# Kernel optimization log

Measured on AMD Instinct MI355X. Metric: run time of the kernel, lower is better.

The kernel has to match this reference:

```python
import jax, jax.numpy as jnp
import numpy as np

NHEAD, HD, ITERS = 8, 32, 6


def _layernorm(x, g, b, eps=1e-5):
    mu = jnp.mean(x, axis=-1, keepdims=True)
    var = jnp.mean((x - mu) ** 2, axis=-1, keepdims=True)
    return g * (x - mu) / jnp.sqrt(var + eps) + b


def _msa1(x, ax, WQ, bQ, WK, bK, WV, bV, WO, bO):
    # ring (sliding-window, size 3) attention + relay node as 4th key/value
    B, L, H = x.shape
    q = (x @ WQ + bQ).reshape(B, L, NHEAD, HD)
    k = (x @ WK + bK).reshape(B, L, NHEAD, HD)
    ak = (ax @ WK + bK).reshape(B, 1, NHEAD, 1, HD)   # relay key
    av = (ax @ WV + bV).reshape(B, 1, NHEAD, 1, HD)   # relay value
    padk = jnp.pad(k, ((0, 0), (1, 1), (0, 0), (0, 0)))
    wins = jnp.stack([padk[:, t:L + t] for t in range(3)], axis=3)  # [B,L,nh,3,hd]
    ak_b = jnp.broadcast_to(ak, (B, L, NHEAD, 1, HD))
    av_b = jnp.broadcast_to(av, (B, L, NHEAD, 1, HD))
    keys = jnp.concatenate([ak_b, wins], axis=3)   # [B,L,nh,4,hd]
    # NOTE: faithful to source bug: window VALUES come from k (pad_v = F.pad(k,...))
    vals = jnp.concatenate([av_b, wins], axis=3)
    scores = jnp.einsum('blnd,blnkd->blnk', q, keys) / np.sqrt(HD).astype(np.float32)
    alphas = jax.nn.softmax(scores, axis=-1)
    att = jnp.einsum('blnk,blnkd->blnd', alphas, vals).reshape(B, L, NHEAD * HD)
    return att @ WO + bO


def _msa2(x, y, WQ, bQ, WK, bK, WV, bV, WO, bO):
    # relay attends over [relay; nodes]; mask arg is ignored in the original
    B, L1, H = y.shape
    q = (x @ WQ + bQ).reshape(B, NHEAD, HD)
    k = (y @ WK + bK).reshape(B, L1, NHEAD, HD)
    v = (y @ WV + bV).reshape(B, L1, NHEAD, HD)
    scores = jnp.einsum('bnd,blnd->bnl', q, k) / np.sqrt(HD).astype(np.float32)
    alphas = jax.nn.softmax(scores, axis=-1)
    att = jnp.einsum('bnl,blnd->bnd', alphas, v).reshape(B, NHEAD * HD)
    return att @ WO + bO


def setup_inputs() -> dict:
    key = jax.random.key(0)
    ks = jax.random.split(key, 32)
    B, L, H, V, E, I = 32, 512, 256, 32000, 300, 6

    def rn(k, shape, s=0.05):
        return jax.random.normal(k, shape, jnp.float32) * s

    inp = {
        'data': jax.random.randint(ks[0], (B, L), 0, V),
        'emb': rn(ks[1], (V, E), 0.1),
        'emb_fc_W': rn(ks[2], (E, H)),
        'emb_fc_b': jnp.zeros((H,), jnp.float32),
        'pos_emb': rn(ks[3], (1000, H), 0.02),
        'ln_g': jnp.ones((I, H), jnp.float32),
        'ln_b': jnp.zeros((I, H), jnp.float32),
    }
    names = ['r_WQ', 'r_WK', 'r_WV', 'r_WO', 's_WQ', 's_WK', 's_WV', 's_WO']
    for j, n in enumerate(names):
        inp[n] = rn(ks[4 + j], (I, H, H))
        inp[n.replace('W', 'b')] = rn(ks[12 + j], (I, H), 0.01)
    return inp


def reference(data, emb, emb_fc_W, emb_fc_b, pos_emb, ln_g, ln_b,
              r_WQ, r_bQ, r_WK, r_bK, r_WV, r_bV, r_WO, r_bO,
              s_WQ, s_bQ, s_WK, s_bK, s_WV, s_bV, s_WO, s_bO):
    B, L = data.shape
    mask = (data == 1)
    e = emb[data]                                  # [B,L,nemb]
    P = pos_emb[:L][None]                          # [1,L,H]
    x0 = e @ emb_fc_W + emb_fc_b + P               # [B,L,H]
    nodes = x0
    relay = jnp.mean(x0, axis=1)                   # [B,H]
    for i in range(ITERS):
        ax = relay
        n_ln = _layernorm(nodes, ln_g[i], ln_b[i])
        nodes = nodes + jax.nn.leaky_relu(
            _msa1(n_ln, ax, r_WQ[i], r_bQ[i], r_WK[i], r_bK[i],
                  r_WV[i], r_bV[i], r_WO[i], r_bO[i]))
        y = jnp.concatenate([relay[:, None, :], nodes], axis=1)
        relay = jax.nn.leaky_relu(
            _msa2(relay, y, s_WQ[i], s_bQ[i], s_WK[i], s_bK[i],
                  s_WV[i], s_bV[i], s_WO[i], s_bO[i]))
        nodes = jnp.where(mask[:, :, None], 0.0, nodes)
    rep = 0.5 * jnp.max(nodes, axis=1) + 0.5 * relay
    return rep
```

## Files before the change

### kernel.cpp

```cpp
#include <hip/hip_runtime.h>
#include <stdint.h>

typedef __bf16 bf16x8 __attribute__((ext_vector_type(8)));
typedef unsigned short ushort8 __attribute__((ext_vector_type(8)));
typedef float floatx4 __attribute__((ext_vector_type(4)));

__device__ __forceinline__ unsigned short f2b(float f) {
    unsigned int u = __builtin_bit_cast(unsigned int, f);
    u += 0x7fffu + ((u >> 16) & 1u);
    return (unsigned short)(u >> 16);
}
__device__ __forceinline__ float b2f(unsigned short u) {
    union { unsigned int i; float f; } x; x.i = ((unsigned int)u) << 16; return x.f;
}

#define SCALE_QK 0.17677669529663687f

__global__ void transpose_many(const float* __restrict__ w0,
                               const float* __restrict__ w1,
                               const float* __restrict__ w2,
                               const float* __restrict__ w3,
                               const float* __restrict__ w4,
                               unsigned short* __restrict__ out) {
    int m = blockIdx.y;
    int fam = m / 6, it = m % 6;
    const float* src =
        (fam == 0 ? w0 : fam == 1 ? w1 : fam == 2 ? w2 : fam == 3 ? w3 : w4) + it * 65536;
    int e = blockIdx.x * 256 + threadIdx.x;
    int n = e >> 8, k = e & 255;
    out[(size_t)(it * 5 + fam) * 65536 + e] = f2b(src[k * 256 + n]);
}

__global__ void transpose_emb(const float* __restrict__ W,
                              unsigned short* __restrict__ out) {
    int e = blockIdx.x * 256 + threadIdx.x;
    int n = e / 320, k = e % 320;
    out[e] = (k < 300) ? f2b(W[k * 256 + n]) : (unsigned short)0;
}

__global__ void gather_emb(const int* __restrict__ data,
                           const float* __restrict__ emb,
                           unsigned short* __restrict__ apad) {
    int row = blockIdx.x;
    int tok = data[row];
    const float* er = emb + (size_t)tok * 300;
    for (int c = threadIdx.x; c < 320; c += 256)
        apad[(size_t)row * 320 + c] = (c < 300) ? f2b(er[c]) : (unsigned short)0;
}

template <int EPI>
__global__ __launch_bounds__(256) void gemm_k(const unsigned short* __restrict__ A, int K,
                                              const unsigned short* __restrict__ Bt,
                                              const float* __restrict__ bias0,
                                              const float* __restrict__ bias1,
                                              float* __restrict__ outF,
                                              unsigned short* __restrict__ outB0,
                                              unsigned short* __restrict__ outB1,
                                              const float* __restrict__ pos,
                                              const int* __restrict__ dmask,
                                              int applyMask) {
    __shared__ unsigned short Asm[64 * 72];
    __shared__ unsigned short Bsm[64 * 72];
    const int tid = threadIdx.x;
    const int wave = tid >> 6, lane = tid & 63;
    const int wm = (wave >> 1) * 32, wn = (wave & 1) * 32;
    const int quad = lane >> 4, l16 = lane & 15;
    const int rowBase = blockIdx.x * 64, colBase = blockIdx.y * 64;
    const int sRow = tid >> 2, sCol = (tid & 3) * 8;
    const unsigned short* aG = A + (size_t)(rowBase + sRow) * K + sCol;
    const unsigned short* bG = Bt + (size_t)(colBase + sRow) * K + sCol;

    floatx4 acc[2][2] = {};
    for (int k0 = 0; k0 < K; k0 += 64) {
        uint4 a0 = *(const uint4*)(aG + k0);
        uint4 a1 = *(const uint4*)(aG + k0 + 32);
        uint4 b0 = *(const uint4*)(bG + k0);
        uint4 b1 = *(const uint4*)(bG + k0 + 32);
        __syncthreads();
        *(uint4*)&Asm[sRow * 72 + sCol] = a0;
        *(uint4*)&Asm[sRow * 72 + sCol + 32] = a1;
        *(uint4*)&Bsm[sRow * 72 + sCol] = b0;
        *(uint4*)&Bsm[sRow * 72 + sCol + 32] = b1;
        __syncthreads();
#pragma unroll
        for (int kk = 0; kk < 64; kk += 32) {
            bf16x8 af0 = __builtin_bit_cast(bf16x8, *(const ushort8*)&Asm[(wm + l16) * 72 + kk + quad * 8]);
            bf16x8 af1 = __builtin_bit_cast(bf16x8, *(const ushort8*)&Asm[(wm + 16 + l16) * 72 + kk + quad * 8]);
            bf16x8 bf0 = __builtin_bit_cast(bf16x8, *(const ushort8*)&Bsm[(wn + l16) * 72 + kk + quad * 8]);
            bf16x8 bf1 = __builtin_bit_cast(bf16x8, *(const ushort8*)&Bsm[(wn + 16 + l16) * 72 + kk + quad * 8]);
            acc[0][0] = __builtin_amdgcn_mfma_f32_16x16x32_bf16(af0, bf0, acc[0][0], 0, 0, 0);
            acc[0][1] = __builtin_amdgcn_mfma_f32_16x16x32_bf16(af0, bf1, acc[0][1], 0, 0, 0);
            acc[1][0] = __builtin_amdgcn_mfma_f32_16x16x32_bf16(af1, bf0, acc[1][0], 0, 0, 0);
            acc[1][1] = __builtin_amdgcn_mfma_f32_16x16x32_bf16(af1, bf1, acc[1][1], 0, 0, 0);
        }
    }
    const int group = colBase >> 8;
    const float* bias = (EPI == 0 && group) ? bias1 : bias0;
    unsigned short* obf = (EPI == 0 && group) ? outB1 : outB0;
#pragma unroll
    for (int tm = 0; tm < 2; tm++) {
#pragma unroll
        for (int tn = 0; tn < 2; tn++) {
            int col = colBase + wn + tn * 16 + l16;
            int lc = col & 255;
            float bv = bias[lc];
#pragma unroll
            for (int r = 0; r < 4; r++) {
                int row = rowBase + wm + tm * 16 + quad * 4 + r;
                float c = acc[tm][tn][r] + bv;
                size_t o = (size_t)row * 256 + lc;
                if (EPI == 0) {
                    obf[o] = f2b(c);
                } else if (EPI == 1) {
                    float v = c > 0.f ? c : 0.01f * c;
                    float base = outF[o];
                    if (applyMask && dmask[row] == 1) base = 0.f;
                    float rr = base + v;
                    outF[o] = rr;
                    outB0[o] = f2b(rr);
                } else {
                    outF[o] = c + pos[(row & 511) * 256 + lc];
                }
            }
        }
    }
}

__global__ void mean_part(const float* __restrict__ nodes, float* __restrict__ part) {
    int b = blockIdx.x, c = blockIdx.y, h = threadIdx.x;
    const float* p = nodes + ((size_t)b * 512 + c * 32) * 256 + h;
    float s = 0.f;
    for (int l = 0; l < 32; l++) s += p[l * 256];
    part[(b * 16 + c) * 256 + h] = s;
}
__global__ void mean_comb(const float* __restrict__ part, float* __restrict__ relay) {
    int b = blockIdx.x, h = threadIdx.x;
    float s = 0.f;
    for (int c = 0; c < 16; c++) s += part[(b * 16 + c) * 256 + h];
    relay[b * 256 + h] = s * (1.f / 512.f);
}

__global__ __launch_bounds__(256) void ln_k(const float* __restrict__ nodes,
                                            const float* __restrict__ g,
                                            const float* __restrict__ bb,
                                            unsigned short* __restrict__ out,
                                            const int* __restrict__ dmask,
                                            int applyMask) {
    __shared__ float red[8];
    int row = blockIdx.x, t = threadIdx.x;
    int wv = t >> 6, ln_ = t & 63;
    float x = nodes[(size_t)row * 256 + t];
    if (applyMask && dmask[row] == 1) x = 0.f;
    float s = x;
#pragma unroll
    for (int o = 32; o; o >>= 1) s += __shfl_xor(s, o);
    if (ln_ == 0) red[wv] = s;
    __syncthreads();
    float mu = (red[0] + red[1] + red[2] + red[3]) * (1.f / 256.f);
    float d = x - mu;
    float v = d * d;
#pragma unroll
    for (int o = 32; o; o >>= 1) v += __shfl_xor(v, o);
    if (ln_ == 0) red[4 + wv] = v;
    __syncthreads();
    float var = (red[4] + red[5] + red[6] + red[7]) * (1.f / 256.f);
    float inv = rsqrtf(var + 1e-5f);
    out[(size_t)row * 256 + t] = f2b(g[t] * d * inv + bb[t]);
}

__global__ void relay5(const float* __restrict__ relay,
                       const float* __restrict__ rWK, const float* __restrict__ rbK,
                       const float* __restrict__ rWV, const float* __restrict__ rbV,
                       const float* __restrict__ sWQ, const float* __restrict__ sbQ,
                       const float* __restrict__ sWK, const float* __restrict__ sbK,
                       const float* __restrict__ sWV, const float* __restrict__ sbV,
                       float* __restrict__ AK, float* __restrict__ AV,
                       float* __restrict__ Q2, float* __restrict__ RK2, float* __restrict__ RV2) {
    __shared__ float r[256];
    int b = blockIdx.x, fam = blockIdx.y, t = threadIdx.x;
    r[t] = relay[b * 256 + t];
    __syncthreads();
    const float* W; const float* bi; float* o;
    switch (fam) {
        case 0: W = rWK; bi = rbK; o = AK; break;
        case 1: W = rWV; bi = rbV; o = AV; break;
        case 2: W = sWQ; bi = sbQ; o = Q2; break;
        case 3: W = sWK; bi = sbK; o = RK2; break;
        default: W = sWV; bi = sbV; o = RV2; break;
    }
    float s = 0.f;
    for (int e = 0; e < 256; e++) s += r[e] * W[e * 256 + t];
    o[b * 256 + t] = s + bi[t];
}

__global__ __launch_bounds__(256) void attn1_k(const unsigned short* __restrict__ q,
                                               const unsigned short* __restrict__ k,
                                               const float* __restrict__ ak,
                                               const float* __restrict__ av,
                                               unsigned short* __restrict__ att) {
    int row = blockIdx.x;
    int b = row >> 9, l = row & 511;
    int t = threadIdx.x;
    size_t o = (size_t)row * 256 + t;
    float qv = b2f(q[o]);
    float k0v = b2f(k[o]);
    float km = (l > 0) ? b2f(k[o - 256]) : 0.f;
    float kp = (l < 511) ? b2f(k[o + 256]) : 0.f;
    float akv = ak[b * 256 + t], avv = av[b * 256 + t];
    float s0 = qv * akv, s1 = qv * km, s2 = qv * k0v, s3 = qv * kp;
#pragma unroll
    for (int off = 16; off; off >>= 1) {
        s0 += __shfl_xor(s0, off, 32);
        s1 += __shfl_xor(s1, off, 32);
        s2 += __shfl_xor(s2, off, 32);
        s3 += __shfl_xor(s3, off, 32);
    }
    s0 *= SCALE_QK; s1 *= SCALE_QK; s2 *= SCALE_QK; s3 *= SCALE_QK;
    float m = fmaxf(fmaxf(s0, s1), fmaxf(s2, s3));
    float e0 = __expf(s0 - m), e1 = __expf(s1 - m), e2 = __expf(s2 - m), e3 = __expf(s3 - m);
    float Z = e0 + e1 + e2 + e3;
    float a = (e0 * avv + e1 * km + e2 * k0v + e3 * kp) / Z;
    att[o] = f2b(a);
}

__global__ __launch_bounds__(256) void attn2_k(const float* __restrict__ q2,
                                               const unsigned short* __restrict__ k2,
                                               const unsigned short* __restrict__ v2,
                                               const float* __restrict__ rk2,
                                               const float* __restrict__ rv2,
                                               float* __restrict__ att2) {
    __shared__ float sc[513];
    __shared__ float qs[32];
    __shared__ float red[16];
    __shared__ float red2[256];
    int bn = blockIdx.x;
    int b = bn >> 3, n = bn & 7;
    int t = threadIdx.x;
    if (t < 32) qs[t] = q2[b * 256 + n * 32 + t];
    __syncthreads();
    float lmax = -1e30f;
    for (int li = t; li < 513; li += 256) {
        float d = 0.f;
        if (li == 0) {
            const float* kr = rk2 + b * 256 + n * 32;
#pragma unroll 8
            for (int j = 0; j < 32; j++) d += qs[j] * kr[j];
        } else {
            const unsigned short* kr = k2 + ((size_t)(b * 512 + li - 1) * 256 + n * 32);
#pragma unroll 8
            for (int j = 0; j < 32; j++) d += qs[j] * b2f(kr[j]);
        }
        d *= SCALE_QK;
        sc[li] = d;
        lmax = fmaxf(lmax, d);
    }
#pragma unroll
    for (int o = 32; o; o >>= 1) lmax = fmaxf(lmax, __shfl_xor(lmax, o));
    if ((t & 63) == 0) red[t >> 6] = lmax;
    __syncthreads();
    float m = fmaxf(fmaxf(red[0], red[1]), fmaxf(red[2], red[3]));
    float lsum = 0.f;
    for (int li = t; li < 513; li += 256) {
        float e = __expf(sc[li] - m);
        sc[li] = e;
        lsum += e;
    }
#pragma unroll
    for (int o = 32; o; o >>= 1) lsum += __shfl_xor(lsum, o);
    if ((t & 63) == 0) red[8 + (t >> 6)] = lsum;
    __syncthreads();
    float Z = red[8] + red[9] + red[10] + red[11];
    int d_ = t & 31, g_ = t >> 5;
    float acc = 0.f;
    for (int li = g_; li < 513; li += 8) {
        if (li == 0) {
            acc += sc[0] * rv2[b * 256 + n * 32 + d_];
        } else {
            acc += sc[li] * b2f(v2[(size_t)(b * 512 + li - 1) * 256 + n * 32 + d_]);
        }
    }
    red2[t] = acc;
    __syncthreads();
    if (t < 32) {
        float s = 0.f;
        for (int g = 0; g < 8; g++) s += red2[g * 32 + t];
        att2[b * 256 + n * 32 + t] = s / Z;
    }
}

__global__ void relay_out2(const float* __restrict__ att2,
                           const float* __restrict__ WO, const float* __restrict__ bO,
                           float* __restrict__ relay) {
    __shared__ float r[256];
    int b = blockIdx.x, t = threadIdx.x;
    r[t] = att2[b * 256 + t];
    __syncthreads();
    float s = 0.f;
    for (int e = 0; e < 256; e++) s += r[e] * WO[e * 256 + t];
    s += bO[t];
    relay[b * 256 + t] = s > 0.f ? s : 0.01f * s;
}

__global__ void rep_part(const float* __restrict__ nodes, const int* __restrict__ dmask,
                         float* __restrict__ part) {
    int b = blockIdx.x, c = blockIdx.y, h = threadIdx.x;
    const float* p = nodes + ((size_t)b * 512 + c * 32) * 256 + h;
    const int* dd = dmask + b * 512 + c * 32;
    float m = -1e30f;
    for (int l = 0; l < 32; l++) {
        float v = (dd[l] == 1) ? 0.f : p[l * 256];
        m = fmaxf(m, v);
    }
    part[(b * 16 + c) * 256 + h] = m;
}
__global__ void rep_comb(const float* __restrict__ part, const float* __restrict__ relay,
                         float* __restrict__ out) {
    int b = blockIdx.x, h = threadIdx.x;
    float m = -1e30f;
    for (int c = 0; c < 16; c++) m = fmaxf(m, part[(b * 16 + c) * 256 + h]);
    out[b * 256 + h] = 0.5f * m + 0.5f * relay[b * 256 + h];
}

extern "C" void kernel_launch(void* const* d_in, const int* in_sizes, int n_in,
                              void* d_out, int out_size, void* d_ws, size_t ws_size,
                              hipStream_t stream) {
    const int* data = (const int*)d_in[0];
    const float* emb = (const float*)d_in[1];
    const float* emb_fc_W = (const float*)d_in[2];
    const float* emb_fc_b = (const float*)d_in[3];
    const float* pos_emb = (const float*)d_in[4];
    const float* ln_g = (const float*)d_in[5];
    const float* ln_b = (const float*)d_in[6];
    const float* r_WQ = (const float*)d_in[7];
    const float* r_bQ = (const float*)d_in[8];
    const float* r_WK = (const float*)d_in[9];
    const float* r_bK = (const float*)d_in[10];
    const float* r_WV = (const float*)d_in[11];
    const float* r_bV = (const float*)d_in[12];
    const float* r_WO = (const float*)d_in[13];
    const float* r_bO = (const float*)d_in[14];
    const float* s_WQ = (const float*)d_in[15];
    const float* s_bQ = (const float*)d_in[16];
    const float* s_WK = (const float*)d_in[17];
    const float* s_bK = (const float*)d_in[18];
    const float* s_WV = (const float*)d_in[19];
    const float* s_bV = (const float*)d_in[20];
    const float* s_WO = (const float*)d_in[21];
    const float* s_bO = (const float*)d_in[22];

    char* w = (char*)d_ws;
    size_t off = 0;
    auto alloc = [&](size_t bytes) -> char* {
        char* p = w + off;
        off += (bytes + 255) & ~(size_t)255;
        return p;
    };
    float* RELAY = (float*)alloc(8192 * 4);
    float* AK = (float*)alloc(8192 * 4);
    float* AV = (float*)alloc(8192 * 4);
    float* Q2 = (float*)alloc(8192 * 4);
    float* RK2 = (float*)alloc(8192 * 4);
    float* RV2 = (float*)alloc(8192 * 4);
    float* ATT2 = (float*)alloc(8192 * 4);
    float* PART = (float*)alloc((size_t)32 * 16 * 256 * 4);
    unsigned short* WTE = (unsigned short*)alloc((size_t)256 * 320 * 2);
    unsigned short* WT = (unsigned short*)alloc((size_t)30 * 65536 * 2);
    float* NODES = (float*)alloc((size_t)16384 * 256 * 4);
    unsigned short* NLN = (unsigned short*)alloc((size_t)16384 * 256 * 2);
    unsigned short* Qb = (unsigned short*)alloc((size_t)16384 * 256 * 2);
    unsigned short* Kb16 = (unsigned short*)alloc((size_t)16384 * 256 * 2);
    unsigned short* NBF = (unsigned short*)alloc((size_t)16384 * 320 * 2);
    unsigned short* AEMB = NBF;
    unsigned short* ATT = NLN;
    unsigned short* K2b = Qb;
    unsigned short* V2b = Kb16;

    transpose_many<<<dim3(256, 30), 256, 0, stream>>>(r_WQ, r_WK, r_WO, s_WK, s_WV, WT);
    transpose_emb<<<320, 256, 0, stream>>>(emb_fc_W, WTE);
    gather_emb<<<16384, 256, 0, stream>>>(data, emb, AEMB);
    gemm_k<2><<<dim3(256, 4), 256, 0, stream>>>(AEMB, 320, WTE, emb_fc_b, nullptr,
                                                NODES, nullptr, nullptr, pos_emb, nullptr, 0);
    mean_part<<<dim3(32, 16), 256, 0, stream>>>(NODES, PART);
    mean_comb<<<32, 256, 0, stream>>>(PART, RELAY);

    for (int i = 0; i < 6; i++) {
        const unsigned short* wQK = WT + (size_t)(i * 5 + 0) * 65536;
        const unsigned short* wO = WT + (size_t)(i * 5 + 2) * 65536;
        const unsigned short* wKV2 = WT + (size_t)(i * 5 + 3) * 65536;

        ln_k<<<16384, 256, 0, stream>>>(NODES, ln_g + i * 256, ln_b + i * 256, NLN, data, i > 0);
        gemm_k<0><<<dim3(256, 8), 256, 0, stream>>>(NLN, 256, wQK, r_bQ + i * 256, r_bK + i * 256,
                                                    nullptr, Qb, Kb16, nullptr, nullptr, 0);
        relay5<<<dim3(32, 5), 256, 0, stream>>>(RELAY,
                                                r_WK + (size_t)i * 65536, r_bK + i * 256,
                                                r_WV + (size_t)i * 65536, r_bV + i * 256,
                                                s_WQ + (size_t)i * 65536, s_bQ + i * 256,
                                                s_WK + (size_t)i * 65536, s_bK + i * 256,
                                                s_WV + (size_t)i * 65536, s_bV + i * 256,
                                                AK, AV, Q2, RK2, RV2);
        attn1_k<<<16384, 256, 0, stream>>>(Qb, Kb16, AK, AV, ATT);
        gemm_k<1><<<dim3(256, 4), 256, 0, stream>>>(ATT, 256, wO, r_bO + i * 256, nullptr,
                                                    NODES, NBF, nullptr, nullptr, data, i > 0);
        gemm_k<0><<<dim3(256, 8), 256, 0, stream>>>(NBF, 256, wKV2, s_bK + i * 256, s_bV + i * 256,
                                                    nullptr, K2b, V2b, nullptr, nullptr, 0);
        attn2_k<<<256, 256, 0, stream>>>(Q2, K2b, V2b, RK2, RV2, ATT2);
        relay_out2<<<32, 256, 0, stream>>>(ATT2, s_WO + (size_t)i * 65536, s_bO + i * 256, RELAY);
    }
    rep_part<<<dim3(32, 16), 256, 0, stream>>>(NODES, data, PART);
    rep_comb<<<32, 256, 0, stream>>>(PART, RELAY, (float*)d_out);
}
```

Before: 858.9 us.

## Load full-K GEMM tiles via direct global-to-LDS with XOR swizzle; vectorize attn1

```diff
diff --git a/kernel.cpp b/kernel.cpp
--- a/kernel.cpp
+++ b/kernel.cpp
@@ -12,6 +12,11 @@
 }
 __device__ __forceinline__ float b2f(unsigned short u) {
     union { unsigned int i; float f; } x; x.i = ((unsigned int)u) << 16; return x.f;
+}
+__device__ __forceinline__ void gl_lds16(const unsigned short* g, unsigned short* l) {
+    __builtin_amdgcn_global_load_lds(
+        (const __attribute__((address_space(1))) unsigned int*)g,
+        (__attribute__((address_space(3))) unsigned int*)l, 16, 0, 0);
 }
 
 #define SCALE_QK 0.17677669529663687f
@@ -48,8 +53,8 @@
         apad[(size_t)row * 320 + c] = (c < 300) ? f2b(er[c]) : (unsigned short)0;
 }
 
-template <int EPI>
-__global__ __launch_bounds__(256) void gemm_k(const unsigned short* __restrict__ A, int K,
+template <int EPI, int KDIM>
+__global__ __launch_bounds__(256) void gemm_k(const unsigned short* __restrict__ A,
                                               const unsigned short* __restrict__ Bt,
                                               const float* __restrict__ bias0,
                                               const float* __restrict__ bias1,
@@ -59,40 +64,45 @@
                                               const float* __restrict__ pos,
                                               const int* __restrict__ dmask,
                                               int applyMask) {
-    __shared__ unsigned short Asm[64 * 72];
-    __shared__ unsigned short Bsm[64 * 72];
+    constexpr int G = KDIM / 8;
+    __shared__ unsigned short Asm[64 * KDIM];
+    __shared__ unsigned short Bsm[64 * KDIM];
     const int tid = threadIdx.x;
     const int wave = tid >> 6, lane = tid & 63;
     const int wm = (wave >> 1) * 32, wn = (wave & 1) * 32;
     const int quad = lane >> 4, l16 = lane & 15;
     const int rowBase = blockIdx.x * 64, colBase = blockIdx.y * 64;
-    const int sRow = tid >> 2, sCol = (tid & 3) * 8;
-    const unsigned short* aG = A + (size_t)(rowBase + sRow) * K + sCol;
-    const unsigned short* bG = Bt + (size_t)(colBase + sRow) * K + sCol;
+
+    {
+        const unsigned short* gbA = A + (size_t)(rowBase + wave * 16) * KDIM;
+        const unsigned short* gbB = Bt + (size_t)(colBase + wave * 16) * KDIM;
+        unsigned short* lbA = Asm + wave * 16 * KDIM;
+        unsigned short* lbB = Bsm + wave * 16 * KDIM;
+#pragma unroll
+        for (int c = 0; c < G / 4; c++) {
+            int gi = c * 64 + lane;
+            int rl = gi / G, sl = gi - rl * G;
+            int sg = sl ^ (rl & 7);
+            gl_lds16(gbA + rl * KDIM + sg * 8, lbA + gi * 8);
+            gl_lds16(gbB + rl * KDIM + sg * 8, lbB + gi * 8);
+        }
+    }
+    __syncthreads();
 
     floatx4 acc[2][2] = {};
-    for (int k0 = 0; k0 < K; k0 += 64) {
-        uint4 a0 = *(const uint4*)(aG + k0);
-        uint4 a1 = *(const uint4*)(aG + k0 + 32);
-        uint4 b0 = *(const uint4*)(bG + k0);
-        uint4 b1 = *(const uint4*)(bG + k0 + 32);
-        __syncthreads();
-        *(uint4*)&Asm[sRow * 72 + sCol] = a0;
-        *(uint4*)&Asm[sRow * 72 + sCol + 32] = a1;
-        *(uint4*)&Bsm[sRow * 72 + sCol] = b0;
-        *(uint4*)&Bsm[sRow * 72 + sCol + 32] = b1;
-        __syncthreads();
-#pragma unroll
-        for (int kk = 0; kk < 64; kk += 32) {
-            bf16x8 af0 = __builtin_bit_cast(bf16x8, *(const ushort8*)&Asm[(wm + l16) * 72 + kk + quad * 8]);
-            bf16x8 af1 = __builtin_bit_cast(bf16x8, *(const ushort8*)&Asm[(wm + 16 + l16) * 72 + kk + quad * 8]);
-            bf16x8 bf0 = __builtin_bit_cast(bf16x8, *(const ushort8*)&Bsm[(wn + l16) * 72 + kk + quad * 8]);
-            bf16x8 bf1 = __builtin_bit_cast(bf16x8, *(const ushort8*)&Bsm[(wn + 16 + l16) * 72 + kk + quad * 8]);
-            acc[0][0] = __builtin_amdgcn_mfma_f32_16x16x32_bf16(af0, bf0, acc[0][0], 0, 0, 0);
-            acc[0][1] = __builtin_amdgcn_mfma_f32_16x16x32_bf16(af0, bf1, acc[0][1], 0, 0, 0);
-            acc[1][0] = __builtin_amdgcn_mfma_f32_16x16x32_bf16(af1, bf0, acc[1][0], 0, 0, 0);
-            acc[1][1] = __builtin_amdgcn_mfma_f32_16x16x32_bf16(af1, bf1, acc[1][1], 0, 0, 0);
-        }
+    const int mr0 = wm + l16, mr1 = wm + 16 + l16;
+    const int nr0 = wn + l16, nr1 = wn + 16 + l16;
+#pragma unroll
+    for (int ks = 0; ks < KDIM / 32; ks++) {
+        int g = ks * 4 + quad;
+        bf16x8 af0 = __builtin_bit_cast(bf16x8, *(const ushort8*)&Asm[mr0 * KDIM + ((g ^ (mr0 & 7)) * 8)]);
+        bf16x8 af1 = __builtin_bit_cast(bf16x8, *(const ushort8*)&Asm[mr1 * KDIM + ((g ^ (mr1 & 7)) * 8)]);
+        bf16x8 bf0 = __builtin_bit_cast(bf16x8, *(const ushort8*)&Bsm[nr0 * KDIM + ((g ^ (nr0 & 7)) * 8)]);
+        bf16x8 bf1 = __builtin_bit_cast(bf16x8, *(const ushort8*)&Bsm[nr1 * KDIM + ((g ^ (nr1 & 7)) * 8)]);
+        acc[0][0] = __builtin_amdgcn_mfma_f32_16x16x32_bf16(af0, bf0, acc[0][0], 0, 0, 0);
+        acc[0][1] = __builtin_amdgcn_mfma_f32_16x16x32_bf16(af0, bf1, acc[0][1], 0, 0, 0);
+        acc[1][0] = __builtin_amdgcn_mfma_f32_16x16x32_bf16(af1, bf0, acc[1][0], 0, 0, 0);
+        acc[1][1] = __builtin_amdgcn_mfma_f32_16x16x32_bf16(af1, bf1, acc[1][1], 0, 0, 0);
     }
     const int group = colBase >> 8;
     const float* bias = (EPI == 0 && group) ? bias1 : bias0;
@@ -198,29 +208,43 @@
                                                const float* __restrict__ ak,
                                                const float* __restrict__ av,
                                                unsigned short* __restrict__ att) {
-    int row = blockIdx.x;
+    int tid = threadIdx.x;
+    int row = blockIdx.x * 4 + (tid >> 6);
     int b = row >> 9, l = row & 511;
-    int t = threadIdx.x;
-    size_t o = (size_t)row * 256 + t;
-    float qv = b2f(q[o]);
-    float k0v = b2f(k[o]);
-    float km = (l > 0) ? b2f(k[o - 256]) : 0.f;
-    float kp = (l < 511) ? b2f(k[o + 256]) : 0.f;
-    float akv = ak[b * 256 + t], avv = av[b * 256 + t];
-    float s0 = qv * akv, s1 = qv * km, s2 = qv * k0v, s3 = qv * kp;
-#pragma unroll
-    for (int off = 16; off; off >>= 1) {
-        s0 += __shfl_xor(s0, off, 32);
-        s1 += __shfl_xor(s1, off, 32);
-        s2 += __shfl_xor(s2, off, 32);
-        s3 += __shfl_xor(s3, off, 32);
+    int t = tid & 63;
+    size_t o = (size_t)row * 256 + t * 4;
+    ushort4 z4; z4.x = z4.y = z4.z = z4.w = 0;
+    ushort4 q4 = *(const ushort4*)(q + o);
+    ushort4 k04 = *(const ushort4*)(k + o);
+    ushort4 km4 = (l > 0) ? *(const ushort4*)(k + o - 256) : z4;
+    ushort4 kp4 = (l < 511) ? *(const ushort4*)(k + o + 256) : z4;
+    float4 akv = *(const float4*)(ak + b * 256 + t * 4);
+    float4 avv = *(const float4*)(av + b * 256 + t * 4);
+    float qv0 = b2f(q4.x), qv1 = b2f(q4.y), qv2 = b2f(q4.z), qv3 = b2f(q4.w);
+    float k00 = b2f(k04.x), k01 = b2f(k04.y), k02 = b2f(k04.z), k03 = b2f(k04.w);
+    float km0 = b2f(km4.x), km1 = b2f(km4.y), km2 = b2f(km4.z), km3 = b2f(km4.w);
+    float kp0 = b2f(kp4.x), kp1 = b2f(kp4.y), kp2 = b2f(kp4.z), kp3 = b2f(kp4.w);
+    float s0 = qv0 * akv.x + qv1 * akv.y + qv2 * akv.z + qv3 * akv.w;
+    float s1 = qv0 * km0 + qv1 * km1 + qv2 * km2 + qv3 * km3;
+    float s2 = qv0 * k00 + qv1 * k01 + qv2 * k02 + qv3 * k03;
+    float s3 = qv0 * kp0 + qv1 * kp1 + qv2 * kp2 + qv3 * kp3;
+#pragma unroll
+    for (int off = 4; off; off >>= 1) {
+        s0 += __shfl_xor(s0, off);
+        s1 += __shfl_xor(s1, off);
+        s2 += __shfl_xor(s2, off);
+        s3 += __shfl_xor(s3, off);
     }
     s0 *= SCALE_QK; s1 *= SCALE_QK; s2 *= SCALE_QK; s3 *= SCALE_QK;
     float m = fmaxf(fmaxf(s0, s1), fmaxf(s2, s3));
     float e0 = __expf(s0 - m), e1 = __expf(s1 - m), e2 = __expf(s2 - m), e3 = __expf(s3 - m);
-    float Z = e0 + e1 + e2 + e3;
-    float a = (e0 * avv + e1 * km + e2 * k0v + e3 * kp) / Z;
-    att[o] = f2b(a);
+    float iZ = 1.f / (e0 + e1 + e2 + e3);
+    ushort4 r4;
+    r4.x = f2b((e0 * avv.x + e1 * km0 + e2 * k00 + e3 * kp0) * iZ);
+    r4.y = f2b((e0 * avv.y + e1 * km1 + e2 * k01 + e3 * kp1) * iZ);
+    r4.z = f2b((e0 * avv.z + e1 * km2 + e2 * k02 + e3 * kp2) * iZ);
+    r4.w = f2b((e0 * avv.w + e1 * km3 + e2 * k03 + e3 * kp3) * iZ);
+    *(ushort4*)(att + o) = r4;
 }
 
 __global__ __launch_bounds__(256) void attn2_k(const float* __restrict__ q2,
@@ -378,8 +402,8 @@
     transpose_many<<<dim3(256, 30), 256, 0, stream>>>(r_WQ, r_WK, r_WO, s_WK, s_WV, WT);
     transpose_emb<<<320, 256, 0, stream>>>(emb_fc_W, WTE);
     gather_emb<<<16384, 256, 0, stream>>>(data, emb, AEMB);
-    gemm_k<2><<<dim3(256, 4), 256, 0, stream>>>(AEMB, 320, WTE, emb_fc_b, nullptr,
-                                                NODES, nullptr, nullptr, pos_emb, nullptr, 0);
+    gemm_k<2, 320><<<dim3(256, 4), 256, 0, stream>>>(AEMB, WTE, emb_fc_b, nullptr,
+                                                     NODES, nullptr, nullptr, pos_emb, nullptr, 0);
     mean_part<<<dim3(32, 16), 256, 0, stream>>>(NODES, PART);
     mean_comb<<<32, 256, 0, stream>>>(PART, RELAY);
 
@@ -389,8 +413,8 @@
         const unsigned short* wKV2 = WT + (size_t)(i * 5 + 3) * 65536;
 
         ln_k<<<16384, 256, 0, stream>>>(NODES, ln_g + i * 256, ln_b + i * 256, NLN, data, i > 0);
-        gemm_k<0><<<dim3(256, 8), 256, 0, stream>>>(NLN, 256, wQK, r_bQ + i * 256, r_bK + i * 256,
-                                                    nullptr, Qb, Kb16, nullptr, nullptr, 0);
+        gemm_k<0, 256><<<dim3(256, 8), 256, 0, stream>>>(NLN, wQK, r_bQ + i * 256, r_bK + i * 256,
+                                                         nullptr, Qb, Kb16, nullptr, nullptr, 0);
         relay5<<<dim3(32, 5), 256, 0, stream>>>(RELAY,
                                                 r_WK + (size_t)i * 65536, r_bK + i * 256,
                                                 r_WV + (size_t)i * 65536, r_bV + i * 256,
@@ -398,11 +422,11 @@
                                                 s_WK + (size_t)i * 65536, s_bK + i * 256,
                                                 s_WV + (size_t)i * 65536, s_bV + i * 256,
                                                 AK, AV, Q2, RK2, RV2);
-        attn1_k<<<16384, 256, 0, stream>>>(Qb, Kb16, AK, AV, ATT);
-        gemm_k<1><<<dim3(256, 4), 256, 0, stream>>>(ATT, 256, wO, r_bO + i * 256, nullptr,
-                                                    NODES, NBF, nullptr, nullptr, data, i > 0);
-        gemm_k<0><<<dim3(256, 8), 256, 0, stream>>>(NBF, 256, wKV2, s_bK + i * 256, s_bV + i * 256,
-                                                    nullptr, K2b, V2b, nullptr, nullptr, 0);
+        attn1_k<<<4096, 256, 0, stream>>>(Qb, Kb16, AK, AV, ATT);
+        gemm_k<1, 256><<<dim3(256, 4), 256, 0, stream>>>(ATT, wO, r_bO + i * 256, nullptr,
+                                                         NODES, NBF, nullptr, nullptr, data, i > 0);
+        gemm_k<0, 256><<<dim3(256, 8), 256, 0, stream>>>(NBF, wKV2, s_bK + i * 256, s_bV + i * 256,
+                                                         nullptr, K2b, V2b, nullptr, nullptr, 0);
         attn2_k<<<256, 256, 0, stream>>>(Q2, K2b, V2b, RK2, RV2, ATT2);
         relay_out2<<<32, 256, 0, stream>>>(ATT2, s_WO + (size_t)i * 65536, s_bO + i * 256, RELAY);
     }
```

Measured after the change: 852.3 us. About the same (-0.8%).
